# Kernel tuning notes

Hardware: AMD Instinct MI355X
Metric: run time of the kernel (lower is better)

The kernel has to match this reference:

```python
import jax, jax.numpy as jnp
import numpy as np

N_NODES = 200000
N_EDGES = 3200000
N_GRAPHS = 1024
NUM_FEATURES = 8


def _glorot(key, shape):
    fan_in, fan_out = shape
    limit = np.sqrt(6.0 / (fan_in + fan_out))
    return jax.random.uniform(key, shape, jnp.float32, -limit, limit)


def setup_inputs() -> dict:
    key = jax.random.key(0)
    ks = jax.random.split(key, 12)
    x = jax.random.normal(ks[0], (N_NODES, NUM_FEATURES), jnp.float32)
    edge_index = jax.random.randint(ks[1], (2, N_EDGES), 0, N_NODES, jnp.int64)
    batch_index = jnp.sort(jax.random.randint(ks[2], (N_NODES,), 0, N_GRAPHS, jnp.int64))
    params = {
        'W0': _glorot(ks[3], (NUM_FEATURES, 64)), 'b0': jnp.zeros((64,), jnp.float32),
        'W1': _glorot(ks[4], (64, 64)),          'b1': jnp.zeros((64,), jnp.float32),
        'W2': _glorot(ks[5], (64, 32)),          'b2': jnp.zeros((32,), jnp.float32),
        'W3': _glorot(ks[6], (32, 32)),          'b3': jnp.zeros((32,), jnp.float32),
        'Wout': _glorot(ks[7], (64, 10)),        'bout': jnp.zeros((10,), jnp.float32),
    }
    return {'x': x, 'edge_index': edge_index, 'batch_index': batch_index, **params}


def _gcn_conv(x, W, b, src, dst, n_nodes):
    """PyG GCNConv: add self-loops, symmetric deg^-1/2 normalization, x@W, scatter-add, +bias."""
    h = x @ W  # [N, out]
    loops = jnp.arange(n_nodes, dtype=src.dtype)
    s = jnp.concatenate([src, loops])
    d = jnp.concatenate([dst, loops])
    ones = jnp.ones_like(d, dtype=h.dtype)
    deg = jax.ops.segment_sum(ones, d, num_segments=n_nodes)  # in-degree incl. self-loop
    dinv = jnp.where(deg > 0, jax.lax.rsqrt(deg), 0.0)
    norm = dinv[s] * dinv[d]  # [E+N]
    msg = h[s] * norm[:, None]  # gather + scale
    agg = jax.ops.segment_sum(msg, d, num_segments=n_nodes)  # scatter-add at target
    return agg + b


def reference(x, edge_index, batch_index, W0, b0, W1, b1, W2, b2, W3, b3, Wout, bout):
    src, dst = edge_index[0], edge_index[1]
    n = x.shape[0]
    h = jnp.tanh(_gcn_conv(x, W0, b0, src, dst, n))
    h = jax.nn.relu(_gcn_conv(h, W1, b1, src, dst, n))
    h = jax.nn.relu(_gcn_conv(h, W2, b2, src, dst, n))
    h = jax.nn.relu(_gcn_conv(h, W3, b3, src, dst, n))
    # global max pool + global mean pool over graphs in the batch
    gmax = jax.ops.segment_max(h, batch_index, num_segments=N_GRAPHS)
    gsum = jax.ops.segment_sum(h, batch_index, num_segments=N_GRAPHS)
    cnt = jax.ops.segment_sum(jnp.ones((n,), h.dtype), batch_index, num_segments=N_GRAPHS)
    gmean = gsum / jnp.maximum(cnt, 1.0)[:, None]
    pooled = jnp.concatenate([gmax, gmean], axis=1)  # [G, 64]
    return pooled @ Wout + bout  # [G, 10]
```

## Files before the change

### kernel.cpp

```cpp
#include <hip/hip_runtime.h>
#include <hip/hip_fp16.h>

#define TPB 256
#define NB_PART 512
#define NB_LOOP 2048

union H8 { float4 f4; __half2 h2[4]; };

__device__ inline void acc_h8(const float4& raw, float* a) {
    H8 u; u.f4 = raw;
#pragma unroll
    for (int i = 0; i < 4; i++) {
        float2 f = __half22float2(u.h2[i]);
        a[2 * i] += f.x;
        a[2 * i + 1] += f.y;
    }
}

__global__ __launch_bounds__(TPB) void k_bhist(const int* __restrict__ dst,
                                               int* __restrict__ bhist, int E, int shift) {
    __shared__ int h[256];
    int tid = threadIdx.x;
    for (int i = tid; i < 256; i += TPB) h[i] = 0;
    __syncthreads();
    int stride = gridDim.x * TPB;
    for (int e = blockIdx.x * TPB + tid; e < E; e += stride)
        atomicAdd(&h[dst[e] >> shift], 1);
    __syncthreads();
    for (int i = tid; i < 256; i += TPB)
        if (h[i]) atomicAdd(&bhist[i], h[i]);
}

__global__ void k_bscan(const int* __restrict__ bhist, int* __restrict__ bstart,
                        int* __restrict__ gcursor, int nbuck) {
    __shared__ int s[256];
    int tid = threadIdx.x;
    int v = bhist[tid];
    s[tid] = v;
    __syncthreads();
    for (int off = 1; off < 256; off <<= 1) {
        int t = (tid >= off) ? s[tid - off] : 0;
        __syncthreads();
        s[tid] += t;
        __syncthreads();
    }
    int excl = s[tid] - v;
    bstart[tid] = excl;
    if (tid == 255) bstart[256] = s[255];
    if (tid < nbuck) gcursor[tid] = excl;
}

__global__ __launch_bounds__(TPB) void k_part(const int* __restrict__ src,
                                              const int* __restrict__ dst,
                                              int* __restrict__ gcursor,
                                              unsigned* __restrict__ staging,
                                              int E, int shift) {
    __shared__ int hist[256];
    __shared__ int base[256];
    int tid = threadIdx.x;
    long long per = (E + gridDim.x - 1) / gridDim.x;
    int e0 = (int)((long long)blockIdx.x * per);
    int e1 = (int)min((long long)E, (long long)e0 + per);
    for (int i = tid; i < 256; i += TPB) hist[i] = 0;
    __syncthreads();
    for (int e = e0 + tid; e < e1; e += TPB) {
        int b = dst[e] >> shift;
        atomicAdd(&hist[b], 1);
    }
    __syncthreads();
    for (int i = tid; i < 256; i += TPB) {
        int c = hist[i];
        base[i] = (c > 0) ? atomicAdd(&gcursor[i], c) : 0;
        hist[i] = 0;
    }
    __syncthreads();
    unsigned lmask = (1u << shift) - 1u;
    for (int e = e0 + tid; e < e1; e += TPB) {
        int d = dst[e];
        int b = d >> shift;
        int p = base[b] + atomicAdd(&hist[b], 1);
        staging[p] = (((unsigned)d & lmask) << 18) | (unsigned)src[e];
    }
}

__global__ __launch_bounds__(TPB) void k_deg_bucket(const unsigned* __restrict__ staging,
                                                    const int* __restrict__ bstart,
                                                    int* __restrict__ deg,
                                                    float* __restrict__ dinv,
                                                    int N, int shift) {
    __shared__ int cnt[4096];
    int b = blockIdx.x;
    int tid = threadIdx.x;
    int base = b << shift;
    int nn = min(1 << shift, N - base);
    for (int i = tid; i < nn; i += TPB) cnt[i] = 0;
    __syncthreads();
    int rs = bstart[b], re = bstart[b + 1];
    for (int j = rs + tid; j < re; j += TPB) atomicAdd(&cnt[staging[j] >> 18], 1);
    __syncthreads();
    for (int i = tid; i < nn; i += TPB) {
        int c = cnt[i];
        deg[base + i] = c;
        dinv[base + i] = rsqrtf((float)c + 1.0f);
    }
}

__global__ __launch_bounds__(TPB) void k_scan1(const int* __restrict__ deg,
                                               int* __restrict__ row_start,
                                               int* __restrict__ bsum, int N) {
    __shared__ int s[TPB];
    int tid = threadIdx.x;
    int i = blockIdx.x * TPB + tid;
    int v = (i < N) ? deg[i] : 0;
    s[tid] = v;
    __syncthreads();
    for (int off = 1; off < TPB; off <<= 1) {
        int t = (tid >= off) ? s[tid - off] : 0;
        __syncthreads();
        s[tid] += t;
        __syncthreads();
    }
    if (i < N) row_start[i] = s[tid] - v;
    if (tid == TPB - 1) bsum[blockIdx.x] = s[tid];
}

__global__ void k_scan2(int* __restrict__ bsum, int nb) {
    __shared__ int s[1024];
    int tid = threadIdx.x;
    int v = (tid < nb) ? bsum[tid] : 0;
    s[tid] = v;
    __syncthreads();
    for (int off = 1; off < 1024; off <<= 1) {
        int t = (tid >= off) ? s[tid - off] : 0;
        __syncthreads();
        s[tid] += t;
        __syncthreads();
    }
    if (tid < nb) bsum[tid] = s[tid] - v;
}

__global__ __launch_bounds__(TPB) void k_scan3(int* __restrict__ row_start,
                                               const int* __restrict__ bsum, int N) {
    int i = blockIdx.x * TPB + threadIdx.x;
    if (i < N) row_start[i] += bsum[blockIdx.x];
}

__global__ __launch_bounds__(TPB) void k_scatter2(const unsigned* __restrict__ staging,
                                                  const int* __restrict__ row_start,
                                                  int* __restrict__ csr,
                                                  int N, int E, int shift) {
    __shared__ int curs[4096];
    int b = blockIdx.x;
    int tid = threadIdx.x;
    int base = b << shift;
    int nn = min(1 << shift, N - base);
    for (int i = tid; i < nn; i += TPB) curs[i] = row_start[base + i];
    __syncthreads();
    int rs = row_start[base];
    int re = (base + nn < N) ? row_start[base + nn] : E;
    for (int j = rs + tid; j < re; j += TPB) {
        unsigned rec = staging[j];
        int s = rec & 0x3FFFF;
        int dl = rec >> 18;
        int p = atomicAdd(&curs[dl], 1);
        csr[p] = s;
    }
}

__global__ __launch_bounds__(TPB) void k_xp16(const float* __restrict__ x,
                                              const float* __restrict__ dinv,
                                              __half* __restrict__ xp, int N) {
    int t = blockIdx.x * TPB + threadIdx.x;
    if (t < N * 8) xp[t] = __float2half(dinv[t >> 3] * x[t]);
}

__global__ __launch_bounds__(TPB) void k_l0fused(const int* __restrict__ row_start,
                                                 const int* __restrict__ deg,
                                                 const int* __restrict__ csr,
                                                 const float* __restrict__ dinv,
                                                 const __half* __restrict__ xp,
                                                 const float* __restrict__ W0,
                                                 const float* __restrict__ b0,
                                                 __half* __restrict__ h0p, int N) {
    int wave = (blockIdx.x * TPB + threadIdx.x) >> 6;
    int lane = threadIdx.x & 63;
    if (wave >= N) return;
    int s0 = row_start[wave], dn = deg[wave];
    const float4* x4 = (const float4*)xp;
    float a[8] = {0, 0, 0, 0, 0, 0, 0, 0};
    for (int j = lane; j < dn; j += 64) acc_h8(x4[csr[s0 + j]], a);
#pragma unroll
    for (int off = 1; off < 64; off <<= 1) {
#pragma unroll
        for (int i = 0; i < 8; i++) a[i] += __shfl_xor(a[i], off, 64);
    }
    float di = dinv[wave];
    H8 u; u.f4 = x4[wave];
    float row[8];
#pragma unroll
    for (int i = 0; i < 4; i++) {
        float2 f = __half22float2(u.h2[i]);
        row[2 * i] = di * (a[2 * i] + f.x);
        row[2 * i + 1] = di * (a[2 * i + 1] + f.y);
    }
    float acc = b0[lane];
#pragma unroll
    for (int k = 0; k < 8; k++) acc += row[k] * W0[k * 64 + lane];
    h0p[(size_t)wave * 64 + lane] = __float2half(di * tanhf(acc));
}

__global__ __launch_bounds__(TPB) void k_pullmm64h(const int* __restrict__ row_start,
                                                   const int* __restrict__ deg,
                                                   const int* __restrict__ csr,
                                                   const float* __restrict__ dinv,
                                                   const __half* __restrict__ h0p,
                                                   const float* __restrict__ W1,
                                                   const float* __restrict__ b1,
                                                   float* __restrict__ h1, int N) {
    __shared__ float Ws[64 * 64];
    __shared__ float rows[4][64];
    int tid = threadIdx.x;
    for (int i = tid; i < 64 * 64; i += TPB) Ws[i] = W1[i];
    __syncthreads();
    int grp = tid >> 6, lane = tid & 63;
    int q = lane & 7, eg = lane >> 3;
    const float4* h4 = (const float4*)h0p;
    int n4 = (N + 3) >> 2;
    for (int blk = blockIdx.x; blk < n4; blk += gridDim.x) {
        int node = blk * 4 + grp;
        if (node < N) {
            int s0 = row_start[node], dn = deg[node];
            float a[8] = {0, 0, 0, 0, 0, 0, 0, 0};
            int j = eg;
            for (; j + 8 < dn; j += 16) {
                int sA = csr[s0 + j];
                int sB = csr[s0 + j + 8];
                float4 vA = h4[(size_t)sA * 8 + q];
                float4 vB = h4[(size_t)sB * 8 + q];
                acc_h8(vA, a);
                acc_h8(vB, a);
            }
            if (j < dn) acc_h8(h4[(size_t)csr[s0 + j] * 8 + q], a);
#pragma unroll
            for (int off = 8; off < 64; off <<= 1) {
#pragma unroll
                for (int i = 0; i < 8; i++) a[i] += __shfl_xor(a[i], off, 64);
            }
            if (eg == 0) {
                float di = dinv[node];
                H8 u; u.f4 = h4[(size_t)node * 8 + q];
#pragma unroll
                for (int i = 0; i < 4; i++) {
                    float2 f = __half22float2(u.h2[i]);
                    rows[grp][q * 8 + 2 * i] = di * (a[2 * i] + f.x);
                    rows[grp][q * 8 + 2 * i + 1] = di * (a[2 * i + 1] + f.y);
                }
            }
            float acc = b1[lane];
#pragma unroll 8
            for (int k = 0; k < 64; k++) acc += rows[grp][k] * Ws[k * 64 + lane];
            h1[(size_t)node * 64 + lane] = fmaxf(acc, 0.0f);
        }
    }
}

__global__ __launch_bounds__(TPB) void k_mmdh(const float* __restrict__ h,
                                              const float* __restrict__ dinv,
                                              const float* __restrict__ W,
                                              __half* __restrict__ out, int N) {
    __shared__ float Ws[64 * 32];
    __shared__ float rows[4][128];
    int tid = threadIdx.x;
    for (int i = tid; i < 64 * 32; i += TPB) Ws[i] = W[i];
    __syncthreads();
    int grp = tid >> 6, lane = tid & 63;
    int which = lane >> 5, f = lane & 31;
    int n8 = (N + 7) >> 3;
    for (int blk = blockIdx.x; blk < n8; blk += gridDim.x) {
        int nbase = blk * 8 + grp * 2;
        if (nbase < N) rows[grp][lane] = h[(size_t)nbase * 64 + lane];
        if (nbase + 1 < N) rows[grp][64 + lane] = h[(size_t)(nbase + 1) * 64 + lane];
        int n = nbase + which;
        if (n < N) {
            float a = 0.0f;
#pragma unroll 8
            for (int k = 0; k < 64; k++) a += rows[grp][which * 64 + k] * Ws[k * 32 + f];
            out[(size_t)n * 32 + f] = __float2half(dinv[n] * a);
        }
    }
}

__global__ __launch_bounds__(TPB) void k_pullfinmm32h(const int* __restrict__ row_start,
                                                      const int* __restrict__ deg,
                                                      const int* __restrict__ csr,
                                                      const float* __restrict__ dinv,
                                                      const __half* __restrict__ t2p,
                                                      const float* __restrict__ b2,
                                                      const float* __restrict__ W3,
                                                      __half* __restrict__ t3p, int N) {
    __shared__ float Ws[32 * 32];
    __shared__ float rows[4][32];
    int tid = threadIdx.x;
    for (int i = tid; i < 32 * 32; i += TPB) Ws[i] = W3[i];
    __syncthreads();
    int grp = tid >> 6, lane = tid & 63;
    int q = lane & 3, eg = lane >> 2;
    const float4* h4 = (const float4*)t2p;
    int n4 = (N + 3) >> 2;
    for (int blk = blockIdx.x; blk < n4; blk += gridDim.x) {
        int node = blk * 4 + grp;
        if (node < N) {
            float di = dinv[node];
            int s0 = row_start[node], dn = deg[node];
            float a[8] = {0, 0, 0, 0, 0, 0, 0, 0};
            int j = eg;
            for (; j + 16 < dn; j += 32) {
                int sA = csr[s0 + j];
                int sB = csr[s0 + j + 16];
                float4 vA = h4[(size_t)sA * 4 + q];
                float4 vB = h4[(size_t)sB * 4 + q];
                acc_h8(vA, a);
                acc_h8(vB, a);
            }
            if (j < dn) acc_h8(h4[(size_t)csr[s0 + j] * 4 + q], a);
#pragma unroll
            for (int off = 4; off < 64; off <<= 1) {
#pragma unroll
                for (int i = 0; i < 8; i++) a[i] += __shfl_xor(a[i], off, 64);
            }
            if (eg == 0) {
                H8 u; u.f4 = h4[(size_t)node * 4 + q];
#pragma unroll
                for (int i = 0; i < 4; i++) {
                    float2 f = __half22float2(u.h2[i]);
                    rows[grp][q * 8 + 2 * i] =
                        fmaxf(di * (a[2 * i] + f.x) + b2[q * 8 + 2 * i], 0.0f);
                    rows[grp][q * 8 + 2 * i + 1] =
                        fmaxf(di * (a[2 * i + 1] + f.y) + b2[q * 8 + 2 * i + 1], 0.0f);
                }
            }
            if (lane < 32) {
                float a2 = 0.0f;
#pragma unroll 8
                for (int k = 0; k < 32; k++) a2 += rows[grp][k] * Ws[k * 32 + lane];
                t3p[(size_t)node * 32 + lane] = __float2half(di * a2);
            }
        }
    }
}

__global__ __launch_bounds__(TPB) void k_pullfin3h(const int* __restrict__ row_start,
                                                   const int* __restrict__ deg,
                                                   const int* __restrict__ csr,
                                                   const float* __restrict__ dinv,
                                                   const __half* __restrict__ t3p,
                                                   const float* __restrict__ b3,
                                                   float* __restrict__ h3, int N) {
    int wave = (blockIdx.x * TPB + threadIdx.x) >> 6;
    int lane = threadIdx.x & 63;
    if (wave >= N) return;
    int q = lane & 3, eg = lane >> 2;
    int s0 = row_start[wave], dn = deg[wave];
    const float4* h4 = (const float4*)t3p;
    float a[8] = {0, 0, 0, 0, 0, 0, 0, 0};
    int j = eg;
    for (; j + 16 < dn; j += 32) {
        int sA = csr[s0 + j];
        int sB = csr[s0 + j + 16];
        float4 vA = h4[(size_t)sA * 4 + q];
        float4 vB = h4[(size_t)sB * 4 + q];
        acc_h8(vA, a);
        acc_h8(vB, a);
    }
    if (j < dn) acc_h8(h4[(size_t)csr[s0 + j] * 4 + q], a);
#pragma unroll
    for (int off = 4; off < 64; off <<= 1) {
#pragma unroll
        for (int i = 0; i < 8; i++) a[i] += __shfl_xor(a[i], off, 64);
    }
    if (eg == 0) {
        float di = dinv[wave];
        H8 u; u.f4 = h4[(size_t)wave * 4 + q];
        float r[8];
#pragma unroll
        for (int i = 0; i < 4; i++) {
            float2 f = __half22float2(u.h2[i]);
            r[2 * i] = fmaxf(di * (a[2 * i] + f.x) + b3[q * 8 + 2 * i], 0.0f);
            r[2 * i + 1] = fmaxf(di * (a[2 * i + 1] + f.y) + b3[q * 8 + 2 * i + 1], 0.0f);
        }
        float4* o = (float4*)h3 + (size_t)wave * 8 + q * 2;
        o[0] = make_float4(r[0], r[1], r[2], r[3]);
        o[1] = make_float4(r[4], r[5], r[6], r[7]);
    }
}

__global__ __launch_bounds__(TPB) void k_gbound(const int* __restrict__ batch,
                                                int* __restrict__ start, int N, int G) {
    int g = blockIdx.x * TPB + threadIdx.x;
    if (g > G) return;
    int lo = 0, hi = N;
    while (lo < hi) {
        int mid = (lo + hi) >> 1;
        if (batch[mid] < g) lo = mid + 1;
        else hi = mid;
    }
    start[g] = lo;
}

__global__ __launch_bounds__(TPB) void k_pool2(const float* __restrict__ h,
                                               const int* __restrict__ start,
                                               float* __restrict__ gmax,
                                               float* __restrict__ gsum, int G) {
    __shared__ float smax[8][32];
    __shared__ float ssum[8][32];
    int g = blockIdx.x;
    int s = start[g], e = start[g + 1];
    int tid = threadIdx.x;
    int nl = tid >> 5, f = tid & 31;
    float mx = 0.0f, sm = 0.0f;
    for (int n = s + nl; n < e; n += 8) {
        float v = h[(size_t)n * 32 + f];
        mx = fmaxf(mx, v);
        sm += v;
    }
    smax[nl][f] = mx;
    ssum[nl][f] = sm;
    __syncthreads();
    if (nl == 0) {
#pragma unroll
        for (int k = 1; k < 8; k++) {
            mx = fmaxf(mx, smax[k][f]);
            sm += ssum[k][f];
        }
        gmax[g * 32 + f] = mx;
        gsum[g * 32 + f] = sm;
    }
}

__global__ __launch_bounds__(TPB) void k_out(const float* __restrict__ gmax,
                                             const float* __restrict__ gsum,
                                             const int* __restrict__ start,
                                             const float* __restrict__ Wout,
                                             const float* __restrict__ bout,
                                             float* __restrict__ out, int G) {
    int t = blockIdx.x * TPB + threadIdx.x;
    if (t >= G * 10) return;
    int g = t / 10, j = t % 10;
    float c = (float)(start[g + 1] - start[g]);
    float inv = 1.0f / fmaxf(c, 1.0f);
    float a = bout[j];
#pragma unroll
    for (int k = 0; k < 32; k++) a += gmax[g * 32 + k] * Wout[k * 10 + j];
#pragma unroll
    for (int k = 0; k < 32; k++) a += (gsum[g * 32 + k] * inv) * Wout[(32 + k) * 10 + j];
    out[t] = a;
}

static inline int cdiv(long long a, int b) { return (int)((a + b - 1) / b); }

extern "C" void kernel_launch(void* const* d_in, const int* in_sizes, int n_in,
                              void* d_out, int out_size, void* d_ws, size_t ws_size,
                              hipStream_t stream) {
    const float* x    = (const float*)d_in[0];
    const int*   ei   = (const int*)d_in[1];
    const int*   bidx = (const int*)d_in[2];
    const float* W0 = (const float*)d_in[3];
    const float* b0 = (const float*)d_in[4];
    const float* W1 = (const float*)d_in[5];
    const float* b1 = (const float*)d_in[6];
    const float* W2 = (const float*)d_in[7];
    const float* b2 = (const float*)d_in[8];
    const float* W3 = (const float*)d_in[9];
    const float* b3 = (const float*)d_in[10];
    const float* Wout = (const float*)d_in[11];
    const float* bout = (const float*)d_in[12];
    float* out = (float*)d_out;

    const int N = in_sizes[0] / 8;
    const int E = in_sizes[1] / 2;
    const int G = out_size / 10;
    const int* src = ei;
    const int* dst = ei + E;

    int shift = 10;
    while (((N + (1 << shift) - 1) >> shift) > 256) shift++;
    const int nbuck = (N + (1 << shift) - 1) >> shift;

    char* w = (char*)d_ws;
    int*   deg_i     = (int*)w;    w += (size_t)N * 4;
    int*   row_start = (int*)w;    w += (size_t)N * 4;
    float* dinv      = (float*)w;  w += (size_t)N * 4;
    float* gmax      = (float*)w;  w += (size_t)G * 32 * 4;
    float* gsum      = (float*)w;  w += (size_t)G * 32 * 4;
    int*   gstart    = (int*)w;    w += (size_t)(G + 4) * 4;
    int*   bhist     = (int*)w;    w += 256 * 4;
    int*   bstart    = (int*)w;    w += 260 * 4;
    int*   csr       = (int*)w;    w += (size_t)E * 4;
    float* bufA      = (float*)w;  w += (size_t)N * 64 * 4;
    float* bufB      = (float*)w;  w += (size_t)N * 64 * 4;
    unsigned* staging = (unsigned*)bufA;
    int*      bsum    = (int*)bufB;
    int*      gcursor = (int*)bufB + 1024;
    __half* xp16  = (__half*)bufB;
    __half* h0p16 = (__half*)bufA;
    float*  h1    = (float*)bufB;
    __half* t2p16 = (__half*)bufA;
    __half* t3p16 = (__half*)bufB;
    float*  h3    = (float*)bufA;

    const int nb = cdiv(N, TPB);

    hipMemsetAsync(bhist, 0, 256 * 4, stream);
    k_bhist<<<256, TPB, 0, stream>>>(dst, bhist, E, shift);
    k_bscan<<<1, 256, 0, stream>>>(bhist, bstart, gcursor, nbuck);
    k_part<<<NB_PART, TPB, 0, stream>>>(src, dst, gcursor, staging, E, shift);
    k_deg_bucket<<<nbuck, TPB, 0, stream>>>(staging, bstart, deg_i, dinv, N, shift);
    k_scan1<<<nb, TPB, 0, stream>>>(deg_i, row_start, bsum, N);
    k_scan2<<<1, 1024, 0, stream>>>(bsum, nb);
    k_scan3<<<nb, TPB, 0, stream>>>(row_start, bsum, N);
    k_scatter2<<<nbuck, TPB, 0, stream>>>(staging, row_start, csr, N, E, shift);
    k_gbound<<<cdiv(G + 1, TPB), TPB, 0, stream>>>(bidx, gstart, N, G);

    k_xp16<<<cdiv((long long)N * 8, TPB), TPB, 0, stream>>>(x, dinv, xp16, N);
    k_l0fused<<<cdiv(N, 4), TPB, 0, stream>>>(row_start, deg_i, csr, dinv, xp16, W0, b0,
                                              h0p16, N);

    k_pullmm64h<<<NB_LOOP, TPB, 0, stream>>>(row_start, deg_i, csr, dinv, h0p16, W1, b1,
                                             h1, N);

    k_mmdh<<<NB_LOOP, TPB, 0, stream>>>(h1, dinv, W2, t2p16, N);
    k_pullfinmm32h<<<NB_LOOP, TPB, 0, stream>>>(row_start, deg_i, csr, dinv, t2p16, b2,
                                                W3, t3p16, N);

    k_pullfin3h<<<cdiv(N, 4), TPB, 0, stream>>>(row_start, deg_i, csr, dinv, t3p16, b3, h3, N);

    k_pool2<<<G, TPB, 0, stream>>>(h3, gstart, gmax, gsum, G);
    k_out<<<cdiv((long long)G * 10, TPB), TPB, 0, stream>>>(gmax, gsum, gstart, Wout, bout,
                                                            out, G);
}
```

Measured before the change: 744.3 us.

## Shrink per-node thread groups in GCN pull kernels and pair-add gathered halves

Layer-0 now assigns 16 lanes per node instead of a full wave, and each lane computes and stores four output features packed as halves. The 32-wide pull kernels for layers 2 and 3 now assign half a wave per node instead of a whole wave, so each wave handles two nodes. With an average in-degree of about 16, this is meant to cut idle lanes and shorten the shuffle reductions. The gather loops also combine two neighbour loads per step, and in the 64-wide layer the pair is added in fp16 before widening, which may lose some precision.

```diff
diff --git a/kernel.cpp b/kernel.cpp
--- a/kernel.cpp
+++ b/kernel.cpp
@@ -6,12 +6,35 @@
 #define NB_LOOP 2048
 
 union H8 { float4 f4; __half2 h2[4]; };
+union U2H4 { uint2 u2; __half2 h2[2]; };
 
 __device__ inline void acc_h8(const float4& raw, float* a) {
     H8 u; u.f4 = raw;
 #pragma unroll
     for (int i = 0; i < 4; i++) {
         float2 f = __half22float2(u.h2[i]);
+        a[2 * i] += f.x;
+        a[2 * i + 1] += f.y;
+    }
+}
+
+__device__ inline void acc_h8x2(const float4& rA, const float4& rB, float* a) {
+    H8 uA, uB; uA.f4 = rA; uB.f4 = rB;
+#pragma unroll
+    for (int i = 0; i < 4; i++) {
+        float2 fA = __half22float2(uA.h2[i]);
+        float2 fB = __half22float2(uB.h2[i]);
+        a[2 * i] += fA.x + fB.x;
+        a[2 * i + 1] += fA.y + fB.y;
+    }
+}
+
+__device__ inline void acc_h8p(const float4& rA, const float4& rB, float* a) {
+    H8 uA, uB; uA.f4 = rA; uB.f4 = rB;
+#pragma unroll
+    for (int i = 0; i < 4; i++) {
+        __half2 s = __hadd2(uA.h2[i], uB.h2[i]);
+        float2 f = __half22float2(s);
         a[2 * i] += f.x;
         a[2 * i + 1] += f.y;
     }
@@ -182,20 +205,21 @@
                                                  const float* __restrict__ W0,
                                                  const float* __restrict__ b0,
                                                  __half* __restrict__ h0p, int N) {
-    int wave = (blockIdx.x * TPB + threadIdx.x) >> 6;
-    int lane = threadIdx.x & 63;
-    if (wave >= N) return;
-    int s0 = row_start[wave], dn = deg[wave];
+    int t = blockIdx.x * TPB + threadIdx.x;
+    int node = t >> 4;
+    int ll = t & 15;
+    if (node >= N) return;
+    int s0 = row_start[node], dn = deg[node];
     const float4* x4 = (const float4*)xp;
     float a[8] = {0, 0, 0, 0, 0, 0, 0, 0};
-    for (int j = lane; j < dn; j += 64) acc_h8(x4[csr[s0 + j]], a);
-#pragma unroll
-    for (int off = 1; off < 64; off <<= 1) {
+    for (int j = ll; j < dn; j += 16) acc_h8(x4[csr[s0 + j]], a);
+#pragma unroll
+    for (int off = 1; off < 16; off <<= 1) {
 #pragma unroll
         for (int i = 0; i < 8; i++) a[i] += __shfl_xor(a[i], off, 64);
     }
-    float di = dinv[wave];
-    H8 u; u.f4 = x4[wave];
+    float di = dinv[node];
+    H8 u; u.f4 = x4[node];
     float row[8];
 #pragma unroll
     for (int i = 0; i < 4; i++) {
@@ -203,10 +227,19 @@
         row[2 * i] = di * (a[2 * i] + f.x);
         row[2 * i + 1] = di * (a[2 * i + 1] + f.y);
     }
-    float acc = b0[lane];
-#pragma unroll
-    for (int k = 0; k < 8; k++) acc += row[k] * W0[k * 64 + lane];
-    h0p[(size_t)wave * 64 + lane] = __float2half(di * tanhf(acc));
+    float o[4];
+#pragma unroll
+    for (int c = 0; c < 4; c++) {
+        int f = ll * 4 + c;
+        float acc = b0[f];
+#pragma unroll
+        for (int k = 0; k < 8; k++) acc += row[k] * W0[k * 64 + f];
+        o[c] = di * tanhf(acc);
+    }
+    U2H4 w;
+    w.h2[0] = __floats2half2_rn(o[0], o[1]);
+    w.h2[1] = __floats2half2_rn(o[2], o[3]);
+    ((uint2*)h0p)[(size_t)node * 16 + ll] = w.u2;
 }
 
 __global__ __launch_bounds__(TPB) void k_pullmm64h(const int* __restrict__ row_start,
@@ -237,8 +270,7 @@
                 int sB = csr[s0 + j + 8];
                 float4 vA = h4[(size_t)sA * 8 + q];
                 float4 vB = h4[(size_t)sB * 8 + q];
-                acc_h8(vA, a);
-                acc_h8(vB, a);
+                acc_h8p(vA, vB, a);
             }
             if (j < dn) acc_h8(h4[(size_t)csr[s0 + j] * 8 + q], a);
 #pragma unroll
@@ -299,32 +331,32 @@
                                                       const float* __restrict__ W3,
                                                       __half* __restrict__ t3p, int N) {
     __shared__ float Ws[32 * 32];
-    __shared__ float rows[4][32];
+    __shared__ float rows[4][2][32];
     int tid = threadIdx.x;
     for (int i = tid; i < 32 * 32; i += TPB) Ws[i] = W3[i];
     __syncthreads();
     int grp = tid >> 6, lane = tid & 63;
-    int q = lane & 3, eg = lane >> 2;
+    int hw = lane >> 5, ll = lane & 31;
+    int q = ll & 3, eg = ll >> 2;
     const float4* h4 = (const float4*)t2p;
-    int n4 = (N + 3) >> 2;
-    for (int blk = blockIdx.x; blk < n4; blk += gridDim.x) {
-        int node = blk * 4 + grp;
+    int n8 = (N + 7) >> 3;
+    for (int blk = blockIdx.x; blk < n8; blk += gridDim.x) {
+        int node = blk * 8 + grp * 2 + hw;
         if (node < N) {
             float di = dinv[node];
             int s0 = row_start[node], dn = deg[node];
             float a[8] = {0, 0, 0, 0, 0, 0, 0, 0};
             int j = eg;
-            for (; j + 16 < dn; j += 32) {
+            for (; j + 8 < dn; j += 16) {
                 int sA = csr[s0 + j];
-                int sB = csr[s0 + j + 16];
+                int sB = csr[s0 + j + 8];
                 float4 vA = h4[(size_t)sA * 4 + q];
                 float4 vB = h4[(size_t)sB * 4 + q];
-                acc_h8(vA, a);
-                acc_h8(vB, a);
+                acc_h8x2(vA, vB, a);
             }
             if (j < dn) acc_h8(h4[(size_t)csr[s0 + j] * 4 + q], a);
 #pragma unroll
-            for (int off = 4; off < 64; off <<= 1) {
+            for (int off = 4; off < 32; off <<= 1) {
 #pragma unroll
                 for (int i = 0; i < 8; i++) a[i] += __shfl_xor(a[i], off, 64);
             }
@@ -333,18 +365,16 @@
 #pragma unroll
                 for (int i = 0; i < 4; i++) {
                     float2 f = __half22float2(u.h2[i]);
-                    rows[grp][q * 8 + 2 * i] =
+                    rows[grp][hw][q * 8 + 2 * i] =
                         fmaxf(di * (a[2 * i] + f.x) + b2[q * 8 + 2 * i], 0.0f);
-                    rows[grp][q * 8 + 2 * i + 1] =
+                    rows[grp][hw][q * 8 + 2 * i + 1] =
                         fmaxf(di * (a[2 * i + 1] + f.y) + b2[q * 8 + 2 * i + 1], 0.0f);
                 }
             }
-            if (lane < 32) {
-                float a2 = 0.0f;
+            float a2 = 0.0f;
 #pragma unroll 8
-                for (int k = 0; k < 32; k++) a2 += rows[grp][k] * Ws[k * 32 + lane];
-                t3p[(size_t)node * 32 + lane] = __float2half(di * a2);
-            }
+            for (int k = 0; k < 32; k++) a2 += rows[grp][hw][k] * Ws[k * 32 + ll];
+            t3p[(size_t)node * 32 + ll] = __float2half(di * a2);
         }
     }
 }
@@ -356,31 +386,31 @@
                                                    const __half* __restrict__ t3p,
                                                    const float* __restrict__ b3,
                                                    float* __restrict__ h3, int N) {
-    int wave = (blockIdx.x * TPB + threadIdx.x) >> 6;
-    int lane = threadIdx.x & 63;
-    if (wave >= N) return;
-    int q = lane & 3, eg = lane >> 2;
-    int s0 = row_start[wave], dn = deg[wave];
+    int t = blockIdx.x * TPB + threadIdx.x;
+    int node = t >> 5;
+    int ll = t & 31;
+    if (node >= N) return;
+    int q = ll & 3, eg = ll >> 2;
+    int s0 = row_start[node], dn = deg[node];
     const float4* h4 = (const float4*)t3p;
     float a[8] = {0, 0, 0, 0, 0, 0, 0, 0};
     int j = eg;
-    for (; j + 16 < dn; j += 32) {
+    for (; j + 8 < dn; j += 16) {
         int sA = csr[s0 + j];
-        int sB = csr[s0 + j + 16];
+        int sB = csr[s0 + j + 8];
         float4 vA = h4[(size_t)sA * 4 + q];
         float4 vB = h4[(size_t)sB * 4 + q];
-        acc_h8(vA, a);
-        acc_h8(vB, a);
+        acc_h8x2(vA, vB, a);
     }
     if (j < dn) acc_h8(h4[(size_t)csr[s0 + j] * 4 + q], a);
 #pragma unroll
-    for (int off = 4; off < 64; off <<= 1) {
+    for (int off = 4; off < 32; off <<= 1) {
 #pragma unroll
         for (int i = 0; i < 8; i++) a[i] += __shfl_xor(a[i], off, 64);
     }
     if (eg == 0) {
-        float di = dinv[wave];
-        H8 u; u.f4 = h4[(size_t)wave * 4 + q];
+        float di = dinv[node];
+        H8 u; u.f4 = h4[(size_t)node * 4 + q];
         float r[8];
 #pragma unroll
         for (int i = 0; i < 4; i++) {
@@ -388,7 +418,7 @@
             r[2 * i] = fmaxf(di * (a[2 * i] + f.x) + b3[q * 8 + 2 * i], 0.0f);
             r[2 * i + 1] = fmaxf(di * (a[2 * i + 1] + f.y) + b3[q * 8 + 2 * i + 1], 0.0f);
         }
-        float4* o = (float4*)h3 + (size_t)wave * 8 + q * 2;
+        float4* o = (float4*)h3 + (size_t)node * 8 + q * 2;
         o[0] = make_float4(r[0], r[1], r[2], r[3]);
         o[1] = make_float4(r[4], r[5], r[6], r[7]);
     }
@@ -522,8 +552,8 @@
     k_gbound<<<cdiv(G + 1, TPB), TPB, 0, stream>>>(bidx, gstart, N, G);
 
     k_xp16<<<cdiv((long long)N * 8, TPB), TPB, 0, stream>>>(x, dinv, xp16, N);
-    k_l0fused<<<cdiv(N, 4), TPB, 0, stream>>>(row_start, deg_i, csr, dinv, xp16, W0, b0,
-                                              h0p16, N);
+    k_l0fused<<<cdiv(N, 16), TPB, 0, stream>>>(row_start, deg_i, csr, dinv, xp16, W0, b0,
+                                               h0p16, N);
 
     k_pullmm64h<<<NB_LOOP, TPB, 0, stream>>>(row_start, deg_i, csr, dinv, h0p16, W1, b1,
                                              h1, N);
@@ -532,7 +562,7 @@
     k_pullfinmm32h<<<NB_LOOP, TPB, 0, stream>>>(row_start, deg_i, csr, dinv, t2p16, b2,
                                                 W3, t3p16, N);
 
-    k_pullfin3h<<<cdiv(N, 4), TPB, 0, stream>>>(row_start, deg_i, csr, dinv, t3p16, b3, h3, N);
+    k_pullfin3h<<<cdiv(N, 8), TPB, 0, stream>>>(row_start, deg_i, csr, dinv, t3p16, b3, h3, N);
 
     k_pool2<<<G, TPB, 0, stream>>>(h3, gstart, gmax, gsum, G);
     k_out<<<cdiv((long long)G * 10, TPB), TPB, 0, stream>>>(gmax, gsum, gstart, Wout, bout,
```

After: 700.8 us. 1.06x faster.
